# Optimization experiments

Measured on AMD Instinct MI355X. Metric: run time of the kernel, lower is better.

The kernel has to match this reference:

```python
import jax, jax.numpy as jnp
import numpy as np

NEG_RATIO = 3

def setup_inputs() -> dict:
    key = jax.random.key(0)
    k1, k2, k3, k4 = jax.random.split(key, 4)
    B, P = 32, 131072
    loc_data = jax.random.normal(k1, (B, P, 4), dtype=jnp.float32)
    conf_data = jax.random.normal(k2, (B, P, 2), dtype=jnp.float32)
    loc_t = jax.random.normal(k3, (B, P, 4), dtype=jnp.float32)
    conf_t = jax.random.randint(k4, (B, P), 0, 2, dtype=jnp.int64)
    return {"loc_data": loc_data, "conf_data": conf_data, "loc_t": loc_t, "conf_t": conf_t}


def reference(loc_data, conf_data, loc_t, conf_t):
    B, P, _ = loc_data.shape
    pos = conf_t > 0                                   # [B, P]
    num_pos = pos.sum(axis=1, keepdims=True)           # [B, 1] per-sample positive count
    N = num_pos.sum().astype(loc_data.dtype)           # total positives (scalar)

    # --- localization loss: smooth L1 over positive priors, mean over selected elems ---
    d = jnp.abs(loc_data - loc_t)
    sl1 = jnp.where(d < 1.0, 0.5 * d * d, d - 0.5)     # [B, P, 4]
    posf = pos.astype(loc_data.dtype)
    # F.smooth_l1_loss(mean over N_pos*4 selected elements), then /= N
    loss_loc = jnp.sum(sl1 * posf[:, :, None]) / (N * 4.0)
    loss_loc = loss_loc / N

    # --- hard negative mining via double argsort rank trick ---
    # score = logsumexp(conf) - conf[gt class]; positives zeroed out
    gathered = jnp.take_along_axis(conf_data, conf_t[:, :, None], axis=2)[:, :, 0]
    score = jax.nn.logsumexp(conf_data, axis=2) - gathered      # [B, P]
    score = jnp.where(pos, jnp.zeros((), score.dtype), score)
    idx_rank = jnp.argsort(jnp.argsort(-score, axis=1), axis=1)  # rank in descending order
    num_neg = jnp.minimum(NEG_RATIO * num_pos, P - 1)            # clamp max=P-1 (no min clamp)
    neg = idx_rank < num_neg                                     # [B, P]

    # --- confidence loss: CE over pos|neg priors, mean over selected, then /= N ---
    sel = (pos | neg).astype(conf_data.dtype)                    # [B, P]
    logp = jax.nn.log_softmax(conf_data, axis=2)                 # [B, P, 2]
    ce = -jnp.take_along_axis(logp, conf_t[:, :, None], axis=2)[:, :, 0]
    loss_conf = jnp.sum(ce * sel) / jnp.sum(sel)
    loss_conf = loss_conf / N

    return (loss_loc, loss_conf)
```

## Files before the change

### kernel.cpp

```cpp
#include <hip/hip_runtime.h>
#include <cstdint>

#define BB 32
#define PP 131072
#define NEG_RATIO 3

struct Ws {
  double sum_sl1;
  double sum_ce_all[BB];
  double sum_ce_pos[BB];
  double ce_neg[BB];
  int    num_pos[BB];
};

__device__ __forceinline__ float sl1f(float a, float b) {
  float d = fabsf(a - b);
  return d < 1.0f ? 0.5f * d * d : d - 0.5f;
}

__device__ __forceinline__ float ce_of(float c0, float c1, int t) {
  float m = fmaxf(c0, c1), mn = fminf(c0, c1);
  float lse = m + log1pf(expf(mn - m));
  return lse - (t ? c1 : c0);
}

__global__ __launch_bounds__(256) void k_main(
    const float4* __restrict__ loc, const float2* __restrict__ conf,
    const float4* __restrict__ loct, const int* __restrict__ conft,
    Ws* __restrict__ ws) {
  const int tid = threadIdx.x;
  const int base = blockIdx.x * 2048;
  const int batch = base >> 17;

  double a_sl1 = 0.0, a_ce_all = 0.0, a_ce_pos = 0.0;
  int a_np = 0;

#pragma unroll
  for (int k = 0; k < 8; ++k) {
    const int i = base + k * 256 + tid;
    const float4 l  = loc[i];
    const float4 lt = loct[i];
    const float2 c  = conf[i];
    const int    t  = conft[i];
    const bool pos = t > 0;

    const float ce = ce_of(c.x, c.y, t);
    a_ce_all += (double)ce;

    const float s = sl1f(l.x, lt.x) + sl1f(l.y, lt.y) +
                    sl1f(l.z, lt.z) + sl1f(l.w, lt.w);
    if (pos) {
      a_ce_pos += (double)ce;
      a_sl1    += (double)s;
      a_np     += 1;
    }
  }

#pragma unroll
  for (int off = 32; off; off >>= 1) {
    a_sl1    += __shfl_down(a_sl1, off);
    a_ce_all += __shfl_down(a_ce_all, off);
    a_ce_pos += __shfl_down(a_ce_pos, off);
    a_np     += __shfl_down(a_np, off);
  }

  __shared__ double s1[4], s2[4], s3[4];
  __shared__ int s4[4];
  const int wave = tid >> 6, lane = tid & 63;
  if (lane == 0) { s1[wave] = a_sl1; s2[wave] = a_ce_all; s3[wave] = a_ce_pos; s4[wave] = a_np; }
  __syncthreads();
  if (tid == 0) {
    atomicAdd(&ws->sum_sl1,           s1[0] + s1[1] + s1[2] + s1[3]);
    atomicAdd(&ws->sum_ce_all[batch], s2[0] + s2[1] + s2[2] + s2[3]);
    atomicAdd(&ws->sum_ce_pos[batch], s3[0] + s3[1] + s3[2] + s3[3]);
    atomicAdd(&ws->num_pos[batch],    s4[0] + s4[1] + s4[2] + s4[3]);
  }
}

__global__ __launch_bounds__(256) void k_select(
    const float2* __restrict__ conf, const int* __restrict__ conft,
    Ws* __restrict__ ws) {
  const int b = blockIdx.x;
  const int npos = ws->num_pos[b];
  const long long M = (long long)PP - npos;
  long long k = (long long)NEG_RATIO * npos;
  if (k > PP - 1) k = PP - 1;
  if (k >= M) return;
  if (k <= 0) return;

  const int tid = threadIdx.x;
  const int rowbase = b * PP;

  __shared__ unsigned hist[2048];
  __shared__ unsigned sh_prefix;
  __shared__ long long sh_kk;

  unsigned prefix = 0;
  long long kk = k;
  const int shifts[3] = {21, 10, 0};
  const int widths[3] = {11, 11, 10};

  for (int pass = 0; pass < 3; ++pass) {
    const int shift = shifts[pass], width = widths[pass];
    const unsigned mask = (1u << width) - 1u;
    for (int j = tid; j < 2048; j += 256) hist[j] = 0;
    __syncthreads();
    for (int i = tid; i < PP; i += 256) {
      const float2 c = conf[rowbase + i];
      const int t = conft[rowbase + i];
      const float score = (t > 0) ? 0.0f : ce_of(c.x, c.y, t);
      const unsigned u = __float_as_uint(score);
      const bool match = (pass == 0) || ((u >> (shift + width)) == prefix);
      if (match) atomicAdd(&hist[(u >> shift) & mask], 1u);
    }
    __syncthreads();
    if (tid == 0) {
      long long c = 0;
      int d = (int)mask;
      for (; d >= 0; --d) {
        c += hist[d];
        if (c >= kk) break;
      }
      if (d < 0) d = 0;
      sh_prefix = (prefix << width) | (unsigned)d;
      sh_kk = kk - (c - (long long)hist[d]);
    }
    __syncthreads();
    prefix = sh_prefix;
    kk = sh_kk;
    __syncthreads();
  }

  const unsigned Tbits = prefix;
  double local_ce = 0.0;
  __shared__ unsigned wavecnt[4];
  __shared__ long long s_rt;
  if (tid == 0) s_rt = 0;
  __syncthreads();
  const int lane = tid & 63, wave = tid >> 6;

  for (int basei = 0; basei < PP; basei += 256) {
    const int i = basei + tid;
    const float2 c = conf[rowbase + i];
    const int t = conft[rowbase + i];
    const float ce = ce_of(c.x, c.y, t);
    const float score = (t > 0) ? 0.0f : ce;
    const unsigned u = __float_as_uint(score);
    const bool gt = u > Tbits;
    const bool eq = (u == Tbits);
    const unsigned long long bal = __ballot(eq ? 1 : 0);
    if (lane == 0) wavecnt[wave] = (unsigned)__popcll(bal);
    __syncthreads();
    long long cross = s_rt;
    for (int w = 0; w < wave; ++w) cross += wavecnt[w];
    const long long myord = cross + __popcll(bal & ((1ULL << lane) - 1ULL));
    if (gt || (eq && myord < kk)) local_ce += (double)ce;
    __syncthreads();
    if (tid == 0) s_rt += (long long)wavecnt[0] + wavecnt[1] + wavecnt[2] + wavecnt[3];
    __syncthreads();
  }

#pragma unroll
  for (int off = 32; off; off >>= 1) local_ce += __shfl_down(local_ce, off);
  __shared__ double s_ce[4];
  if (lane == 0) s_ce[wave] = local_ce;
  __syncthreads();
  if (tid == 0) ws->ce_neg[b] = s_ce[0] + s_ce[1] + s_ce[2] + s_ce[3];
}

__global__ __launch_bounds__(64) void k_final(const Ws* __restrict__ ws,
                                              float* __restrict__ out) {
  const int tid = threadIdx.x;
  double np_d = 0.0, ce_sel = 0.0, cnt = 0.0;
  if (tid < BB) {
    const int npos = ws->num_pos[tid];
    const long long M = (long long)PP - npos;
    long long k = (long long)NEG_RATIO * npos;
    if (k > PP - 1) k = PP - 1;
    np_d = (double)npos;
    if (k >= M) {
      ce_sel = ws->sum_ce_all[tid];
      cnt = (double)PP;
    } else {
      const long long kc = k > 0 ? k : 0;
      ce_sel = ws->sum_ce_pos[tid] + ws->ce_neg[tid];
      cnt = (double)(npos + kc);
    }
  }
#pragma unroll
  for (int off = 32; off; off >>= 1) {
    np_d   += __shfl_down(np_d, off);
    ce_sel += __shfl_down(ce_sel, off);
    cnt    += __shfl_down(cnt, off);
  }
  if (tid == 0) {
    const double N = np_d;
    const double S = ws->sum_sl1;
    out[0] = (float)(S / (4.0 * N * N));
    out[1] = (float)(ce_sel / cnt / N);
  }
}

extern "C" void kernel_launch(void* const* d_in, const int* in_sizes, int n_in,
                              void* d_out, int out_size, void* d_ws, size_t ws_size,
                              hipStream_t stream) {
  const float4* loc  = (const float4*)d_in[0];
  const float2* conf = (const float2*)d_in[1];
  const float4* loct = (const float4*)d_in[2];
  const int*    cnft = (const int*)d_in[3];
  Ws* ws = (Ws*)d_ws;

  hipMemsetAsync(d_ws, 0, sizeof(Ws), stream);
  k_main<<<dim3((BB * PP) / 2048), dim3(256), 0, stream>>>(loc, conf, loct, cnft, ws);
  k_select<<<dim3(BB), dim3(256), 0, stream>>>(conf, cnft, ws);
  k_final<<<dim3(1), dim3(64), 0, stream>>>(ws, (float*)d_out);
}
```

Measured before the change: 200.5 us.

## Use float accumulators, vectorized loads and fast math in main reduction kernel

Rewrites k_main so each thread handles four consecutive priors with wide float4/int4 loads, computes CE with fast exp/log intrinsics, and accumulates in float instead of double. The per-sample loc-loss sum becomes a per-batch float array, reduced in k_final. This targets FP64 arithmetic, double shuffles and double atomics in the streaming kernel, and doubles the block count. Float accumulation and fast intrinsics may lose precision. The k_select kernel, which is likely a large part of the runtime, is unchanged.

```diff
diff --git a/kernel.cpp b/kernel.cpp
--- a/kernel.cpp
+++ b/kernel.cpp
@@ -6,16 +6,28 @@
 #define NEG_RATIO 3
 
 struct Ws {
-  double sum_sl1;
-  double sum_ce_all[BB];
-  double sum_ce_pos[BB];
-  double ce_neg[BB];
-  int    num_pos[BB];
+  float sum_sl1[BB];
+  float sum_ce_all[BB];
+  float sum_ce_pos[BB];
+  float ce_neg[BB];
+  int   num_pos[BB];
 };
 
-__device__ __forceinline__ float sl1f(float a, float b) {
-  float d = fabsf(a - b);
-  return d < 1.0f ? 0.5f * d * d : d - 0.5f;
+__device__ __forceinline__ float sl1sum(float4 a, float4 b) {
+  float dx = fabsf(a.x - b.x), dy = fabsf(a.y - b.y),
+        dz = fabsf(a.z - b.z), dw = fabsf(a.w - b.w);
+  float sx = dx < 1.0f ? 0.5f * dx * dx : dx - 0.5f;
+  float sy = dy < 1.0f ? 0.5f * dy * dy : dy - 0.5f;
+  float sz = dz < 1.0f ? 0.5f * dz * dz : dz - 0.5f;
+  float sw = dw < 1.0f ? 0.5f * dw * dw : dw - 0.5f;
+  return (sx + sy) + (sz + sw);
+}
+
+__device__ __forceinline__ float ce_fast(float c0, float c1, int t) {
+  float m = fmaxf(c0, c1);
+  float d = fabsf(c0 - c1);
+  float lse = m + __logf(1.0f + __expf(-d));
+  return lse - (t ? c1 : c0);
 }
 
 __device__ __forceinline__ float ce_of(float c0, float c1, int t) {
@@ -25,36 +37,34 @@
 }
 
 __global__ __launch_bounds__(256) void k_main(
-    const float4* __restrict__ loc, const float2* __restrict__ conf,
-    const float4* __restrict__ loct, const int* __restrict__ conft,
+    const float4* __restrict__ loc, const float4* __restrict__ conf2,
+    const float4* __restrict__ loct, const int4* __restrict__ conft4,
     Ws* __restrict__ ws) {
-  const int tid = threadIdx.x;
-  const int base = blockIdx.x * 2048;
-  const int batch = base >> 17;
-
-  double a_sl1 = 0.0, a_ce_all = 0.0, a_ce_pos = 0.0;
-  int a_np = 0;
-
-#pragma unroll
-  for (int k = 0; k < 8; ++k) {
-    const int i = base + k * 256 + tid;
-    const float4 l  = loc[i];
-    const float4 lt = loct[i];
-    const float2 c  = conf[i];
-    const int    t  = conft[i];
-    const bool pos = t > 0;
-
-    const float ce = ce_of(c.x, c.y, t);
-    a_ce_all += (double)ce;
-
-    const float s = sl1f(l.x, lt.x) + sl1f(l.y, lt.y) +
-                    sl1f(l.z, lt.z) + sl1f(l.w, lt.w);
-    if (pos) {
-      a_ce_pos += (double)ce;
-      a_sl1    += (double)s;
-      a_np     += 1;
-    }
-  }
+  const int gtid = blockIdx.x * 256 + threadIdx.x;
+  const int batch = blockIdx.x >> 7;
+  const int p0 = gtid * 4;
+
+  const float4 l0 = loc[p0 + 0], l1 = loc[p0 + 1], l2 = loc[p0 + 2], l3 = loc[p0 + 3];
+  const float4 t0 = loct[p0 + 0], t1 = loct[p0 + 1], t2 = loct[p0 + 2], t3 = loct[p0 + 3];
+  const float4 ca = conf2[gtid * 2 + 0];
+  const float4 cb = conf2[gtid * 2 + 1];
+  const int4   tt = conft4[gtid];
+
+  const float ce0 = ce_fast(ca.x, ca.y, tt.x);
+  const float ce1 = ce_fast(ca.z, ca.w, tt.y);
+  const float ce2 = ce_fast(cb.x, cb.y, tt.z);
+  const float ce3 = ce_fast(cb.z, cb.w, tt.w);
+
+  const float s0 = sl1sum(l0, t0), s1 = sl1sum(l1, t1),
+              s2 = sl1sum(l2, t2), s3 = sl1sum(l3, t3);
+
+  const float m0 = tt.x > 0 ? 1.0f : 0.0f, m1 = tt.y > 0 ? 1.0f : 0.0f,
+              m2 = tt.z > 0 ? 1.0f : 0.0f, m3 = tt.w > 0 ? 1.0f : 0.0f;
+
+  float a_ce_all = (ce0 + ce1) + (ce2 + ce3);
+  float a_ce_pos = (m0 * ce0 + m1 * ce1) + (m2 * ce2 + m3 * ce3);
+  float a_sl1    = (m0 * s0 + m1 * s1) + (m2 * s2 + m3 * s3);
+  int   a_np     = (tt.x > 0) + (tt.y > 0) + (tt.z > 0) + (tt.w > 0);
 
 #pragma unroll
   for (int off = 32; off; off >>= 1) {
@@ -64,16 +74,16 @@
     a_np     += __shfl_down(a_np, off);
   }
 
-  __shared__ double s1[4], s2[4], s3[4];
-  __shared__ int s4[4];
-  const int wave = tid >> 6, lane = tid & 63;
-  if (lane == 0) { s1[wave] = a_sl1; s2[wave] = a_ce_all; s3[wave] = a_ce_pos; s4[wave] = a_np; }
+  __shared__ float s1s[4], s2s[4], s3s[4];
+  __shared__ int s4s[4];
+  const int wave = threadIdx.x >> 6, lane = threadIdx.x & 63;
+  if (lane == 0) { s1s[wave] = a_sl1; s2s[wave] = a_ce_all; s3s[wave] = a_ce_pos; s4s[wave] = a_np; }
   __syncthreads();
-  if (tid == 0) {
-    atomicAdd(&ws->sum_sl1,           s1[0] + s1[1] + s1[2] + s1[3]);
-    atomicAdd(&ws->sum_ce_all[batch], s2[0] + s2[1] + s2[2] + s2[3]);
-    atomicAdd(&ws->sum_ce_pos[batch], s3[0] + s3[1] + s3[2] + s3[3]);
-    atomicAdd(&ws->num_pos[batch],    s4[0] + s4[1] + s4[2] + s4[3]);
+  if (threadIdx.x == 0) {
+    atomicAdd(&ws->sum_sl1[batch],    (s1s[0] + s1s[1]) + (s1s[2] + s1s[3]));
+    atomicAdd(&ws->sum_ce_all[batch], (s2s[0] + s2s[1]) + (s2s[2] + s2s[3]));
+    atomicAdd(&ws->sum_ce_pos[batch], (s3s[0] + s3s[1]) + (s3s[2] + s3s[3]));
+    atomicAdd(&ws->num_pos[batch],     s4s[0] + s4s[1] + s4s[2] + s4s[3]);
   }
 }
 
@@ -165,25 +175,26 @@
   __shared__ double s_ce[4];
   if (lane == 0) s_ce[wave] = local_ce;
   __syncthreads();
-  if (tid == 0) ws->ce_neg[b] = s_ce[0] + s_ce[1] + s_ce[2] + s_ce[3];
+  if (tid == 0) ws->ce_neg[b] = (float)(s_ce[0] + s_ce[1] + s_ce[2] + s_ce[3]);
 }
 
 __global__ __launch_bounds__(64) void k_final(const Ws* __restrict__ ws,
                                               float* __restrict__ out) {
   const int tid = threadIdx.x;
-  double np_d = 0.0, ce_sel = 0.0, cnt = 0.0;
+  double np_d = 0.0, ce_sel = 0.0, cnt = 0.0, sl1 = 0.0;
   if (tid < BB) {
     const int npos = ws->num_pos[tid];
     const long long M = (long long)PP - npos;
     long long k = (long long)NEG_RATIO * npos;
     if (k > PP - 1) k = PP - 1;
     np_d = (double)npos;
+    sl1 = (double)ws->sum_sl1[tid];
     if (k >= M) {
-      ce_sel = ws->sum_ce_all[tid];
+      ce_sel = (double)ws->sum_ce_all[tid];
       cnt = (double)PP;
     } else {
       const long long kc = k > 0 ? k : 0;
-      ce_sel = ws->sum_ce_pos[tid] + ws->ce_neg[tid];
+      ce_sel = (double)ws->sum_ce_pos[tid] + (double)ws->ce_neg[tid];
       cnt = (double)(npos + kc);
     }
   }
@@ -192,11 +203,11 @@
     np_d   += __shfl_down(np_d, off);
     ce_sel += __shfl_down(ce_sel, off);
     cnt    += __shfl_down(cnt, off);
+    sl1    += __shfl_down(sl1, off);
   }
   if (tid == 0) {
     const double N = np_d;
-    const double S = ws->sum_sl1;
-    out[0] = (float)(S / (4.0 * N * N));
+    out[0] = (float)(sl1 / (4.0 * N * N));
     out[1] = (float)(ce_sel / cnt / N);
   }
 }
@@ -204,14 +215,16 @@
 extern "C" void kernel_launch(void* const* d_in, const int* in_sizes, int n_in,
                               void* d_out, int out_size, void* d_ws, size_t ws_size,
                               hipStream_t stream) {
-  const float4* loc  = (const float4*)d_in[0];
-  const float2* conf = (const float2*)d_in[1];
-  const float4* loct = (const float4*)d_in[2];
-  const int*    cnft = (const int*)d_in[3];
+  const float4* loc   = (const float4*)d_in[0];
+  const float4* conf2 = (const float4*)d_in[1];
+  const float2* conf  = (const float2*)d_in[1];
+  const float4* loct  = (const float4*)d_in[2];
+  const int*    cnft  = (const int*)d_in[3];
+  const int4*   cnft4 = (const int4*)d_in[3];
   Ws* ws = (Ws*)d_ws;
 
   hipMemsetAsync(d_ws, 0, sizeof(Ws), stream);
-  k_main<<<dim3((BB * PP) / 2048), dim3(256), 0, stream>>>(loc, conf, loct, cnft, ws);
+  k_main<<<dim3((BB * PP) / 1024), dim3(256), 0, stream>>>(loc, conf2, loct, cnft4, ws);
   k_select<<<dim3(BB), dim3(256), 0, stream>>>(conf, cnft, ws);
   k_final<<<dim3(1), dim3(64), 0, stream>>>(ws, (float*)d_out);
 }
```

Result: faster. 194.6 us (-3.0%).
